# Kernel tuning notes

Hardware: AMD Instinct MI355X
Metric: run time of the kernel (lower is better)

Reference implementation:

```python
import jax, jax.numpy as jnp
import numpy as np

B, NC, CH, HF, WF = 2, 6, 256, 32, 88
N, CIN = 100000, 128
VOXEL_SIZE = jnp.array([0.075, 0.075, 0.2], dtype=jnp.float32)
PC_MIN = jnp.array([-54.0, -54.0, -5.0], dtype=jnp.float32)
DOWNSAMPLE = 8.0
DMIN, DMAX = 1.0, 60.0


def setup_inputs() -> dict:
    key = jax.random.key(0)
    ks = jax.random.split(key, 12)
    # voxel coords: (batch, z, y, x), batch column sorted to match the
    # original per-batch-loop concatenation order
    b = jnp.repeat(jnp.arange(B, dtype=jnp.int32), N // B)
    x = jax.random.randint(ks[0], (N,), 0, 1440, dtype=jnp.int32)
    y = jax.random.randint(ks[1], (N,), 0, 1440, dtype=jnp.int32)
    z = jax.random.randint(ks[2], (N,), 0, 40, dtype=jnp.int32)
    voxel_coords = jnp.stack([b, z, y, x], axis=1)
    voxel_features = jax.random.normal(ks[3], (N, CIN), dtype=jnp.float32)
    img_feats = jax.random.normal(ks[4], (B, NC, CH, HF, WF), dtype=jnp.float32)
    # pinhole intrinsics for a 704x256 image
    K = jnp.array([[500.0, 0.0, 352.0], [0.0, 500.0, 128.0], [0.0, 0.0, 1.0]], dtype=jnp.float32)
    intrins = K + 0.01 * jax.random.normal(ks[5], (B, NC, 3, 3), dtype=jnp.float32)
    post_rots = 0.5 * jnp.eye(3, dtype=jnp.float32) + 0.001 * jax.random.normal(ks[6], (B, NC, 3, 3), dtype=jnp.float32)
    post_trans = 0.01 * jax.random.normal(ks[7], (B, NC, 3), dtype=jnp.float32)
    # bda: near-identity 4x4
    bda = jnp.tile(jnp.eye(4, dtype=jnp.float32), (B, 1, 1))
    bda = bda.at[:, :3, :3].add(0.01 * jax.random.normal(ks[8], (B, 3, 3), dtype=jnp.float32))
    bda = bda.at[:, :3, 3].set(0.1 * jax.random.normal(ks[9], (B, 3), dtype=jnp.float32))
    # lidar->cam: standard axis permutation (x->z) so depth is positive for half the scene
    R = jnp.array([[0.0, -1.0, 0.0], [0.0, 0.0, -1.0], [1.0, 0.0, 0.0]], dtype=jnp.float32)
    l2c = jnp.tile(jnp.eye(4, dtype=jnp.float32), (B, NC, 1, 1))
    l2c = l2c.at[..., :3, :3].set(R + 0.01 * jax.random.normal(ks[10], (B, NC, 3, 3), dtype=jnp.float32))
    l2c = l2c.at[..., :3, 3].set(0.1 * jax.random.normal(ks[11], (B, NC, 3), dtype=jnp.float32))
    W = 0.02 * jax.random.normal(jax.random.fold_in(key, 99), (CIN, CH), dtype=jnp.float32)
    return dict(voxel_features=voxel_features, voxel_coords=voxel_coords, img_feats=img_feats,
                intrins=intrins, post_rots=post_rots, post_trans=post_trans, bda=bda,
                lidar2cam=l2c, W=W)


def reference(voxel_features, voxel_coords, img_feats, intrins, post_rots, post_trans, bda, lidar2cam, W):
    bidx = voxel_coords[:, 0]
    # voxel index (x,y,z) -> metric lidar coords
    p = voxel_coords[:, jnp.array([3, 2, 1])].astype(jnp.float32) * VOXEL_SIZE + PC_MIN  # [N,3]
    # undo bda augmentation: (p - t) @ inv(R).T
    binv = jnp.linalg.inv(bda[:, :3, :3])  # [B,3,3]
    pcam = jnp.einsum('nj,nij->ni', p - bda[bidx, :3, 3], binv[bidx])  # [N,3]
    # lidar2img = cam2img @ lidar2cam.T (faithful to original, incl. full 4x4 transpose)
    cam2img = jnp.tile(jnp.eye(4, dtype=intrins.dtype), (B, NC, 1, 1)).at[..., :3, :3].set(intrins)
    L = cam2img @ jnp.swapaxes(lidar2cam, -1, -2)  # [B,NC,4,4]
    Lv = L[bidx]  # [N,NC,4,4]
    pimg = jnp.einsum('nj,ncij->nci', pcam, Lv[:, :, :3, :3]) + Lv[:, :, :3, 3]  # [N,NC,3]
    pimg = jnp.concatenate([pimg[..., :2] / pimg[..., 2:3], pimg[..., 2:3]], axis=-1)
    pimg = jnp.einsum('ncj,ncij->nci', pimg, post_rots[bidx]) + post_trans[bidx]
    # gather_img_feature: round/clip + masked gather, scatter into zeros == multiply by mask
    coor = jnp.round(pimg[..., :2] / DOWNSAMPLE)
    depth = pimg[..., 2]
    mask = ((coor[..., 0] >= 0) & (coor[..., 0] < WF) & (coor[..., 1] >= 0) & (coor[..., 1] < HF)
            & (depth < DMAX) & (depth >= DMIN))  # [N,NC]
    xi = jnp.clip(coor[..., 0].astype(jnp.int32), 0, WF - 1)
    yi = jnp.clip(coor[..., 1].astype(jnp.int32), 0, HF - 1)
    cams = jnp.arange(NC)[None, :]
    g = img_feats[bidx[:, None], cams, :, yi, xi]  # [N,NC,CH]
    g = g * mask[..., None].astype(g.dtype)
    # sum over cameras, then Linear(256 -> CIN, no bias)
    img_voxel = jnp.einsum('nc,oc->no', g.sum(axis=1), W)  # [N,CIN]
    out_feats = jnp.concatenate([voxel_features, img_voxel], axis=0)  # [2N,CIN]
    out_coords = jnp.concatenate([voxel_coords, voxel_coords], axis=0)  # [2N,4]
    return out_feats, out_coords
```

## Files before the change

### kernel.cpp

```cpp
#include <hip/hip_runtime.h>
#include <math.h>

#define BB   2
#define NCAM 6
#define CH   256
#define COUT 128
#define HF   32
#define WF   88
#define NPIX (BB * NCAM * HF * WF)
#define NV   100000
#define CIN  128
#define VPB  40

typedef __attribute__((ext_vector_type(8))) short short8;
typedef __attribute__((ext_vector_type(4))) float f32x4;

static __device__ inline short f2bf(float f) {
    union { float f; unsigned u; } v; v.f = f;
    unsigned r = (v.u + 0x7fffu + ((v.u >> 16) & 1u)) >> 16;
    return (short)r;
}
static __device__ inline float bflo(unsigned int pk) {
    union { unsigned int u; float f; } a; a.u = pk << 16; return a.f;
}
static __device__ inline float bfhi(unsigned int pk) {
    union { unsigned int u; float f; } a; a.u = pk & 0xffff0000u; return a.f;
}

__global__ void prep_params_w(const float* __restrict__ intrins,
                              const float* __restrict__ post_rots,
                              const float* __restrict__ post_trans,
                              const float* __restrict__ bda,
                              const float* __restrict__ l2c,
                              const float* __restrict__ W,
                              double* __restrict__ params,
                              short*  __restrict__ Wbf)
{
    if (blockIdx.x > 0) {
        int chunk = blockIdx.x - 1;
        int l = threadIdx.x;
        int nt = chunk >> 3, kk = chunk & 7;
        int n = nt * 16 + (l & 15);
        int k = kk * 32 + (l >> 4) * 8;
        short v[8];
        #pragma unroll
        for (int j = 0; j < 8; j++) v[j] = f2bf(W[n * CH + k + j]);
        *(short8*)(Wbf + ((size_t)chunk * 64 + l) * 8) = *(short8*)v;
        return;
    }

    int t = threadIdx.x;
    if (t >= BB * NCAM) return;
    int b = t / NCAM;

    const float* Bm = bda + b * 16;
    double a00 = Bm[0], a01 = Bm[1], a02 = Bm[2],  tx = Bm[3];
    double a10 = Bm[4], a11 = Bm[5], a12 = Bm[6],  ty = Bm[7];
    double a20 = Bm[8], a21 = Bm[9], a22 = Bm[10], tz = Bm[11];

    double det = a00*(a11*a22 - a12*a21) - a01*(a10*a22 - a12*a20) + a02*(a10*a21 - a11*a20);
    double id  = 1.0 / det;
    double inv[3][3];
    inv[0][0] =  (a11*a22 - a12*a21) * id;
    inv[0][1] = -(a01*a22 - a02*a21) * id;
    inv[0][2] =  (a01*a12 - a02*a11) * id;
    inv[1][0] = -(a10*a22 - a12*a20) * id;
    inv[1][1] =  (a00*a22 - a02*a20) * id;
    inv[1][2] = -(a00*a12 - a02*a10) * id;
    inv[2][0] =  (a10*a21 - a11*a20) * id;
    inv[2][1] = -(a00*a21 - a01*a20) * id;
    inv[2][2] =  (a00*a11 - a01*a10) * id;

    const float* In = intrins + t * 9;
    const float* Lc = l2c + t * 16;

    double M3[3][3];
    #pragma unroll
    for (int i = 0; i < 3; i++)
        #pragma unroll
        for (int j = 0; j < 3; j++)
            M3[i][j] = (double)In[i*3+0] * (double)Lc[j*4+0]
                     + (double)In[i*3+1] * (double)Lc[j*4+1]
                     + (double)In[i*3+2] * (double)Lc[j*4+2];

    double M[3][3];
    #pragma unroll
    for (int i = 0; i < 3; i++)
        #pragma unroll
        for (int j = 0; j < 3; j++)
            M[i][j] = M3[i][0]*inv[0][j] + M3[i][1]*inv[1][j] + M3[i][2]*inv[2][j];

    double* P = params + t * 24;
    #pragma unroll
    for (int i = 0; i < 3; i++)
        #pragma unroll
        for (int j = 0; j < 3; j++)
            P[i*3+j] = M[i][j];
    #pragma unroll
    for (int i = 0; i < 3; i++)
        P[9+i] = -(M[i][0]*tx + M[i][1]*ty + M[i][2]*tz);
    #pragma unroll
    for (int i = 0; i < 9; i++) P[12+i] = (double)post_rots[t*9 + i];
    #pragma unroll
    for (int i = 0; i < 3; i++) P[21+i] = (double)post_trans[t*3 + i];
}

__global__ __launch_bounds__(256) void pixel_mm(const float* __restrict__ img,
                                                const short* __restrict__ Wbf,
                                                unsigned short* __restrict__ imgP)
{
    const int w    = (blockIdx.x << 2) + (threadIdx.x >> 6);
    const int lane = threadIdx.x & 63;
    const int bc   = w / 176;
    const int pt   = w - bc * 176;
    const int pix0 = pt * 16;

    const float* A0 = img + (size_t)bc * (CH * HF * WF) + pix0 + (lane & 15);
    const int q8 = (lane >> 4) * 8;

    f32x4 acc[8];
    #pragma unroll
    for (int nt = 0; nt < 8; nt++) acc[nt] = (f32x4){0.f, 0.f, 0.f, 0.f};

    const short8* Bf = (const short8*)Wbf;
    for (int kk = 0; kk < 8; kk++) {
        short av[8];
        #pragma unroll
        for (int j = 0; j < 8; j++)
            av[j] = f2bf(A0[(size_t)(kk * 32 + q8 + j) * (HF * WF)]);
        short8 a = *(short8*)av;
        #pragma unroll
        for (int nt = 0; nt < 8; nt++)
            acc[nt] = __builtin_amdgcn_mfma_f32_16x16x32_bf16(
                          a, Bf[(nt * 8 + kk) * 64 + lane], acc[nt], 0, 0, 0);
    }

    const int col = lane & 15, rq = lane >> 4;
    unsigned short* P0 = imgP + ((size_t)bc * (HF * WF) + pix0 + rq * 4) * COUT + col;
    #pragma unroll
    for (int nt = 0; nt < 8; nt++)
        #pragma unroll
        for (int r = 0; r < 4; r++)
            P0[(size_t)r * COUT + nt * 16] = (unsigned short)f2bf(acc[nt][r]);
}

struct POF { int o; float m; };

__global__ __launch_bounds__(256) void voxel_gather(
    const float*          __restrict__ vf,
    const int*            __restrict__ coords,
    const unsigned short* __restrict__ imgP,
    const double*         __restrict__ params,
    float*                __restrict__ out)
{
    const int t  = threadIdx.x;
    const int n0 = blockIdx.x * VPB;

    {
        const float4* vf4 = (const float4*)vf;
        float4*       o4  = (float4*)out;
        int base = n0 * (CIN / 4);
        #pragma unroll
        for (int i = 0; i < 5; i++)
            o4[base + i * 256 + t] = vf4[base + i * 256 + t];
    }
    if (t < VPB * 4) {
        int gi = n0 * 4 + t;
        float cv = (float)coords[gi];
        const size_t cb = (size_t)2 * NV * CIN;
        out[cb + gi]                  = cv;
        out[cb + (size_t)NV * 4 + gi] = cv;
    }

    __shared__ POF pof[VPB][NCAM];

    if (t < VPB * NCAM) {
        int vi = t / NCAM, c = t - vi * NCAM;
        int n  = n0 + vi;
        int b  = coords[n * 4 + 0];
        int zi = coords[n * 4 + 1];
        int yi = coords[n * 4 + 2];
        int xi = coords[n * 4 + 3];
        double px = (double)xi * (double)0.075f + (-54.0);
        double py = (double)yi * (double)0.075f + (-54.0);
        double pz = (double)zi * (double)0.2f   + (-5.0);
        const double* P = params + (b * NCAM + c) * 24;
        double X = P[0]*px + P[1]*py + P[2]*pz + P[9];
        double Y = P[3]*px + P[4]*py + P[5]*pz + P[10];
        double Z = P[6]*px + P[7]*py + P[8]*pz + P[11];
        double u = X / Z;
        double v = Y / Z;
        double q0 = P[12]*u + P[13]*v + P[14]*Z + P[21];
        double q1 = P[15]*u + P[16]*v + P[17]*Z + P[22];
        double q2 = P[18]*u + P[19]*v + P[20]*Z + P[23];
        double cx = rint(q0 * 0.125);
        double cy = rint(q1 * 0.125);
        bool m = (cx >= 0.0) && (cx < (double)WF) && (cy >= 0.0) && (cy < (double)HF)
              && (q2 < 60.0) && (q2 >= 1.0);
        int o = 0;
        if (m) {
            int ix = (int)cx, iy = (int)cy;
            o = ((b * NCAM + c) * HF + iy) * WF + ix;
        }
        POF p2; p2.o = o; p2.m = m ? 1.0f : 0.0f;
        pof[vi][c] = p2;
    }
    __syncthreads();

    const int h = t >> 5, l32 = t & 31;
    #pragma unroll
    for (int vv = 0; vv < 5; vv++) {
        int vi = h * 5 + vv;
        float a0 = 0.f, a1 = 0.f, a2 = 0.f, a3 = 0.f;
        #pragma unroll
        for (int c = 0; c < NCAM; c++) {
            POF p2 = pof[vi][c];
            if (p2.m != 0.0f) {
                const unsigned short* px = imgP + (size_t)p2.o * COUT + l32 * 4;
                uint2 A = *(const uint2*)px;
                a0 += bflo(A.x); a1 += bfhi(A.x);
                a2 += bflo(A.y); a3 += bfhi(A.y);
            }
        }
        float4 r4 = {a0, a1, a2, a3};
        *(float4*)(out + ((size_t)NV + n0 + vi) * CIN + l32 * 4) = r4;
    }
}

extern "C" void kernel_launch(void* const* d_in, const int* in_sizes, int n_in,
                              void* d_out, int out_size, void* d_ws, size_t ws_size,
                              hipStream_t stream)
{
    const float* vf      = (const float*)d_in[0];
    const int*   coords  = (const int*)d_in[1];
    const float* img     = (const float*)d_in[2];
    const float* intrins = (const float*)d_in[3];
    const float* prots   = (const float*)d_in[4];
    const float* ptrans  = (const float*)d_in[5];
    const float* bda     = (const float*)d_in[6];
    const float* l2c     = (const float*)d_in[7];
    const float* W       = (const float*)d_in[8];
    float* out = (float*)d_out;

    double* params = (double*)d_ws;
    const size_t wbf_off  = 4096;
    const size_t wbf_sz   = (size_t)8 * 8 * 64 * 8 * sizeof(short);
    const size_t imgP_off = wbf_off + wbf_sz;

    short*          Wbf  = (short*)((char*)d_ws + wbf_off);
    unsigned short* imgP = (unsigned short*)((char*)d_ws + imgP_off);

    prep_params_w<<<65, 64, 0, stream>>>(intrins, prots, ptrans, bda, l2c, W, params, Wbf);
    pixel_mm<<<(12 * 176) / 4, 256, 0, stream>>>(img, Wbf, imgP);
    voxel_gather<<<NV / VPB, 256, 0, stream>>>(vf, coords, imgP, params, out);
}
```

Before: 210.7 us.

## Split pixel GEMM output columns across warps and use nontemporal streaming stores

pixel_mm now assigns one 16-pixel tile per block, and each of the four warps computes two of the eight 16-column output tiles. This gives four times as many blocks, with fewer accumulators and more latency hiding per warp. The cost is that each warp redundantly loads and converts the same A fragment, so image reads from L2 go up. voxel_gather also switches its streaming copies and output writes to nontemporal loads and stores, to avoid polluting the cache that the imgP gathers rely on.

```diff
diff --git a/kernel.cpp b/kernel.cpp
--- a/kernel.cpp
+++ b/kernel.cpp
@@ -109,39 +109,41 @@
                                                 const short* __restrict__ Wbf,
                                                 unsigned short* __restrict__ imgP)
 {
-    const int w    = (blockIdx.x << 2) + (threadIdx.x >> 6);
     const int lane = threadIdx.x & 63;
-    const int bc   = w / 176;
-    const int pt   = w - bc * 176;
+    const int w    = threadIdx.x >> 6;
+    const int bc   = blockIdx.x / 176;
+    const int pt   = blockIdx.x - bc * 176;
     const int pix0 = pt * 16;
 
     const float* A0 = img + (size_t)bc * (CH * HF * WF) + pix0 + (lane & 15);
     const int q8 = (lane >> 4) * 8;
-
-    f32x4 acc[8];
-    #pragma unroll
-    for (int nt = 0; nt < 8; nt++) acc[nt] = (f32x4){0.f, 0.f, 0.f, 0.f};
+    const int nt0 = 2 * w;
+
+    f32x4 acc[2];
+    acc[0] = (f32x4){0.f, 0.f, 0.f, 0.f};
+    acc[1] = (f32x4){0.f, 0.f, 0.f, 0.f};
 
     const short8* Bf = (const short8*)Wbf;
+    #pragma unroll
     for (int kk = 0; kk < 8; kk++) {
         short av[8];
         #pragma unroll
         for (int j = 0; j < 8; j++)
             av[j] = f2bf(A0[(size_t)(kk * 32 + q8 + j) * (HF * WF)]);
         short8 a = *(short8*)av;
-        #pragma unroll
-        for (int nt = 0; nt < 8; nt++)
-            acc[nt] = __builtin_amdgcn_mfma_f32_16x16x32_bf16(
-                          a, Bf[(nt * 8 + kk) * 64 + lane], acc[nt], 0, 0, 0);
+        acc[0] = __builtin_amdgcn_mfma_f32_16x16x32_bf16(
+                     a, Bf[((nt0)     * 8 + kk) * 64 + lane], acc[0], 0, 0, 0);
+        acc[1] = __builtin_amdgcn_mfma_f32_16x16x32_bf16(
+                     a, Bf[((nt0 + 1) * 8 + kk) * 64 + lane], acc[1], 0, 0, 0);
     }
 
     const int col = lane & 15, rq = lane >> 4;
     unsigned short* P0 = imgP + ((size_t)bc * (HF * WF) + pix0 + rq * 4) * COUT + col;
     #pragma unroll
-    for (int nt = 0; nt < 8; nt++)
+    for (int nt = 0; nt < 2; nt++)
         #pragma unroll
         for (int r = 0; r < 4; r++)
-            P0[(size_t)r * COUT + nt * 16] = (unsigned short)f2bf(acc[nt][r]);
+            P0[(size_t)r * COUT + (nt0 + nt) * 16] = (unsigned short)f2bf(acc[nt][r]);
 }
 
 struct POF { int o; float m; };
@@ -157,19 +159,21 @@
     const int n0 = blockIdx.x * VPB;
 
     {
-        const float4* vf4 = (const float4*)vf;
-        float4*       o4  = (float4*)out;
+        const f32x4* vf4 = (const f32x4*)vf;
+        f32x4*       o4  = (f32x4*)out;
         int base = n0 * (CIN / 4);
         #pragma unroll
-        for (int i = 0; i < 5; i++)
-            o4[base + i * 256 + t] = vf4[base + i * 256 + t];
+        for (int i = 0; i < 5; i++) {
+            f32x4 v = __builtin_nontemporal_load(vf4 + base + i * 256 + t);
+            __builtin_nontemporal_store(v, o4 + base + i * 256 + t);
+        }
     }
     if (t < VPB * 4) {
         int gi = n0 * 4 + t;
         float cv = (float)coords[gi];
         const size_t cb = (size_t)2 * NV * CIN;
-        out[cb + gi]                  = cv;
-        out[cb + (size_t)NV * 4 + gi] = cv;
+        __builtin_nontemporal_store(cv, out + cb + gi);
+        __builtin_nontemporal_store(cv, out + cb + (size_t)NV * 4 + gi);
     }
 
     __shared__ POF pof[VPB][NCAM];
@@ -222,8 +226,9 @@
                 a2 += bflo(A.y); a3 += bfhi(A.y);
             }
         }
-        float4 r4 = {a0, a1, a2, a3};
-        *(float4*)(out + ((size_t)NV + n0 + vi) * CIN + l32 * 4) = r4;
+        f32x4 r4 = {a0, a1, a2, a3};
+        __builtin_nontemporal_store(r4,
+            (f32x4*)(out + ((size_t)NV + n0 + vi) * CIN + l32 * 4));
     }
 }
 
@@ -251,6 +256,6 @@
     unsigned short* imgP = (unsigned short*)((char*)d_ws + imgP_off);
 
     prep_params_w<<<65, 64, 0, stream>>>(intrins, prots, ptrans, bda, l2c, W, params, Wbf);
-    pixel_mm<<<(12 * 176) / 4, 256, 0, stream>>>(img, Wbf, imgP);
+    pixel_mm<<<12 * 176, 256, 0, stream>>>(img, Wbf, imgP);
     voxel_gather<<<NV / VPB, 256, 0, stream>>>(vf, coords, imgP, params, out);
 }
```

New measurement: 216.8 us. 1.03x slower.

## Split pixel_mm K dimension across wave pairs with LDS reduction

Applied to the files above, without the earlier changes.

Each pixel tile is now computed by two waves that each handle half of the 256-channel reduction, and the partial accumulators are exchanged through shared memory so each wave writes half of the output columns. All fp32 image loads for a wave's K-half are issued up front before any MFMA, to expose more memory-level parallelism. This doubles the block count and shortens each wave's serial load chain. The cost is a shared-memory buffer, a block-wide barrier, and higher register pressure from the prefetched values.

```diff
diff --git a/kernel.cpp b/kernel.cpp
--- a/kernel.cpp
+++ b/kernel.cpp
@@ -109,39 +109,63 @@
                                                 const short* __restrict__ Wbf,
                                                 unsigned short* __restrict__ imgP)
 {
-    const int w    = (blockIdx.x << 2) + (threadIdx.x >> 6);
-    const int lane = threadIdx.x & 63;
-    const int bc   = w / 176;
-    const int pt   = w - bc * 176;
+    const int t    = threadIdx.x;
+    const int lane = t & 63;
+    const int w    = t >> 6;
+    const int tw   = w & 1;
+    const int kh   = w >> 1;
+    const int tile = blockIdx.x * 2 + tw;
+    const int bc   = tile / 176;
+    const int pt   = tile - bc * 176;
     const int pix0 = pt * 16;
 
     const float* A0 = img + (size_t)bc * (CH * HF * WF) + pix0 + (lane & 15);
     const int q8 = (lane >> 4) * 8;
 
+    float af[4][8];
+    #pragma unroll
+    for (int k2 = 0; k2 < 4; k2++)
+        #pragma unroll
+        for (int j = 0; j < 8; j++)
+            af[k2][j] = A0[(size_t)((kh * 4 + k2) * 32 + q8 + j) * (HF * WF)];
+
     f32x4 acc[8];
     #pragma unroll
     for (int nt = 0; nt < 8; nt++) acc[nt] = (f32x4){0.f, 0.f, 0.f, 0.f};
 
     const short8* Bf = (const short8*)Wbf;
-    for (int kk = 0; kk < 8; kk++) {
+    #pragma unroll
+    for (int k2 = 0; k2 < 4; k2++) {
         short av[8];
         #pragma unroll
-        for (int j = 0; j < 8; j++)
-            av[j] = f2bf(A0[(size_t)(kk * 32 + q8 + j) * (HF * WF)]);
+        for (int j = 0; j < 8; j++) av[j] = f2bf(af[k2][j]);
         short8 a = *(short8*)av;
+        const int kk = kh * 4 + k2;
         #pragma unroll
         for (int nt = 0; nt < 8; nt++)
             acc[nt] = __builtin_amdgcn_mfma_f32_16x16x32_bf16(
                           a, Bf[(nt * 8 + kk) * 64 + lane], acc[nt], 0, 0, 0);
     }
 
+    __shared__ f32x4 red[2][8][64];
+    const int keep0 = kh * 4;
+    #pragma unroll
+    for (int i = 0; i < 4; i++) {
+        int nt = (keep0 ^ 4) + i;
+        red[tw][nt][lane] = acc[nt];
+    }
+    __syncthreads();
+
     const int col = lane & 15, rq = lane >> 4;
     unsigned short* P0 = imgP + ((size_t)bc * (HF * WF) + pix0 + rq * 4) * COUT + col;
     #pragma unroll
-    for (int nt = 0; nt < 8; nt++)
+    for (int i = 0; i < 4; i++) {
+        int nt = keep0 + i;
+        f32x4 s = acc[nt] + red[tw][nt][lane];
         #pragma unroll
         for (int r = 0; r < 4; r++)
-            P0[(size_t)r * COUT + nt * 16] = (unsigned short)f2bf(acc[nt][r]);
+            P0[(size_t)r * COUT + nt * 16] = (unsigned short)f2bf(s[r]);
+    }
 }
 
 struct POF { int o; float m; };
@@ -251,6 +275,6 @@
     unsigned short* imgP = (unsigned short*)((char*)d_ws + imgP_off);
 
     prep_params_w<<<65, 64, 0, stream>>>(intrins, prots, ptrans, bda, l2c, W, params, Wbf);
-    pixel_mm<<<(12 * 176) / 4, 256, 0, stream>>>(img, Wbf, imgP);
+    pixel_mm<<<(12 * 176) / 2, 256, 0, stream>>>(img, Wbf, imgP);
     voxel_gather<<<NV / VPB, 256, 0, stream>>>(vf, coords, imgP, params, out);
 }
```

After: 223.8 us. 1.06x slower.
